# Optimization experiments

Hardware: AMD Instinct MI355X
Metric: run time of the kernel (lower is better)

## Reference

```python
import jax, jax.numpy as jnp
import numpy as np

TEMP = 0.07
DIAG_FILL = -10.0


def setup_inputs() -> dict:
    key = jax.random.key(0)
    k1, k2 = jax.random.split(key)
    N, D = 8192, 256
    feat_q = jax.random.normal(k1, (N, D), dtype=jnp.float32)
    feat_k = jax.random.normal(k2, (N, D), dtype=jnp.float32)
    return {"feat_q": feat_q, "feat_k": feat_k}


def reference(feat_q, feat_k):
    # feat_k is detached in the original module
    feat_k = jax.lax.stop_gradient(feat_k)
    N = feat_q.shape[0]

    q_norm = jnp.linalg.norm(feat_q, axis=-1, keepdims=True)  # [N,1]
    k_norm = jnp.linalg.norm(feat_k, axis=-1, keepdims=True)  # [N,1]

    # positive logits: cosine similarity of matching patches -> [N,1]
    l_pos = jnp.sum(feat_q * feat_k, axis=-1, keepdims=True) / (q_norm * k_norm)

    # negative logits: pairwise cosine similarities -> [N,N]
    l_neg = jnp.einsum('nd,md->nm', feat_q, feat_k) / (q_norm * k_norm.T)
    # mask diagonal (self pairs) with -10.0
    diag = jnp.eye(N, dtype=bool)
    l_neg = jnp.where(diag, jnp.float32(DIAG_FILL), l_neg)

    out = jnp.concatenate([l_pos, l_neg], axis=1) / TEMP  # [N, 1+N]
    # cross-entropy with target class 0, reduction='none'
    loss = jax.nn.logsumexp(out, axis=1) - out[:, 0]
    return loss
```

## Files before the change

kernel.cpp:

```cpp
#include <hip/hip_runtime.h>
#include <stdint.h>

#define N_ROWS 8192
#define DIM 256

constexpr float INV_T = 1.0f / 0.07f;
constexpr float M0    = 1.0f / 0.07f;
constexpr float LOG2E = 1.44269504088896f;
constexpr float C1    = INV_T * LOG2E;
constexpr float C0    = -M0 * LOG2E;
constexpr float KSCL  = 127.0f / 0.35f;

typedef int i32x4  __attribute__((ext_vector_type(4)));
typedef int i32x16 __attribute__((ext_vector_type(16)));

__device__ inline float fast_exp2(float x) {
    float r;
    asm("v_exp_f32 %0, %1" : "=v"(r) : "v"(x));
    return r;
}
__device__ inline int pack4(int a, int b, int c, int d) {
    return (a & 0xff) | ((b & 0xff) << 8) | ((c & 0xff) << 16) | (d << 24);
}

__global__ __launch_bounds__(256) void prep_kernel(
    const float* __restrict__ q, const float* __restrict__ k,
    int* __restrict__ qi8, int* __restrict__ ki8,
    float* __restrict__ lposT, float* __restrict__ fqs) {
    const int wid  = threadIdx.x >> 6;
    const int lane = threadIdx.x & 63;
    const int row  = blockIdx.x * 4 + wid;

    const float4 qv = *reinterpret_cast<const float4*>(q + (size_t)row * DIM + lane * 4);
    const float4 kv = *reinterpret_cast<const float4*>(k + (size_t)row * DIM + lane * 4);

    float qq = qv.x*qv.x + qv.y*qv.y + qv.z*qv.z + qv.w*qv.w;
    float kk = kv.x*kv.x + kv.y*kv.y + kv.z*kv.z + kv.w*kv.w;
    float qk = qv.x*kv.x + qv.y*kv.y + qv.z*kv.z + qv.w*kv.w;
    float qm = fmaxf(fmaxf(fabsf(qv.x), fabsf(qv.y)), fmaxf(fabsf(qv.z), fabsf(qv.w)));

    #pragma unroll
    for (int off = 32; off > 0; off >>= 1) {
        qq += __shfl_xor(qq, off, 64);
        kk += __shfl_xor(kk, off, 64);
        qk += __shfl_xor(qk, off, 64);
        qm  = fmaxf(qm, __shfl_xor(qm, off, 64));
    }
    const float iq = 1.0f / sqrtf(qq);
    const float ik = 1.0f / sqrtf(kk);

    const float ksc = ik * KSCL;
    int k0 = __float2int_rn(fminf(fmaxf(kv.x * ksc, -127.f), 127.f));
    int k1 = __float2int_rn(fminf(fmaxf(kv.y * ksc, -127.f), 127.f));
    int k2 = __float2int_rn(fminf(fmaxf(kv.z * ksc, -127.f), 127.f));
    int k3 = __float2int_rn(fminf(fmaxf(kv.w * ksc, -127.f), 127.f));
    ki8[(size_t)row * 64 + lane] = pack4(k0, k1, k2, k3);

    const float qsc = 127.0f / qm;
    int q0 = __float2int_rn(qv.x * qsc);
    int q1 = __float2int_rn(qv.y * qsc);
    int q2 = __float2int_rn(qv.z * qsc);
    int q3 = __float2int_rn(qv.w * qsc);
    qi8[(size_t)row * 64 + lane] = pack4(q0, q1, q2, q3);

    if (lane == 0) {
        lposT[row] = qk * iq * ik * INV_T;
        fqs[row] = C1 * (0.35f / (127.0f * 127.0f)) * qm * iq;
    }
}

__global__ __launch_bounds__(256, 3) void gemm_lse_kernel(
    const uint8_t* __restrict__ qi8, const uint8_t* __restrict__ ki8,
    const float* __restrict__ fqs, float* __restrict__ ps) {
    __shared__ char lds[3 * 8192];

    const int tid  = threadIdx.x;
    const int lane = tid & 63;
    const int wid  = tid >> 6;
    const int l31  = lane & 31;
    const int l5   = lane >> 5;

    const int qtile = blockIdx.x;
    const int strip = blockIdx.y;
    const int qw    = qtile * 256 + wid * 64;
    const int ks0   = strip * 512;

    auto stage = [&](int t) {
        char* dst = lds + (t % 3) * 8192;
        const int kr0 = ks0 + t * 32;
        #pragma unroll
        for (int s = 0; s < 2; ++s) {
            const int n    = wid * 2 + s;
            const int lrow = n * 8 + (lane >> 3);
            const int row  = lrow & 31;
            const int h    = lrow >> 5;
            const uint8_t* gp = ki8 + (size_t)(kr0 + row) * 256 + h * 128
                              + (((lane & 7) ^ (lrow & 7)) << 4);
            __builtin_amdgcn_global_load_lds(
                (const __attribute__((address_space(1))) void*)gp,
                (__attribute__((address_space(3))) void*)(dst + n * 1024),
                16, 0, 0);
        }
    };

    i32x4 qf[8][2];
    #pragma unroll
    for (int ks = 0; ks < 8; ++ks)
        #pragma unroll
        for (int cg = 0; cg < 2; ++cg)
            qf[ks][cg] = *reinterpret_cast<const i32x4*>(
                qi8 + (size_t)(qw + cg * 32 + l31) * 256 + ks * 32 + l5 * 16);
    const float f0 = fqs[qw + l31];
    const float f1 = fqs[qw + 32 + l31];

    stage(0);
    stage(1);

    i32x16 acc0 = {}, acc1 = {};
    float ssum0 = 0.f, ssum1 = 0.f;

    auto lda = [&](const char* src, i32x4* a) {
        #pragma unroll
        for (int ks = 0; ks < 8; ++ks) {
            const int o    = ks * 32 + l5 * 16;
            const int lrow = l31 + ((o >> 7) << 5);
            const int slot = ((o & 127) >> 4) ^ (lrow & 7);
            a[ks] = *reinterpret_cast<const i32x4*>(src + lrow * 128 + (slot << 4));
        }
    };

    auto expfrag = [&](i32x16& A, bool diag, float f, float& ss) {
        float s = 0.f;
        #pragma unroll
        for (int r = 0; r < 16; ++r) {
            float e = fast_exp2(fmaf((float)A[r], f, C0));
            if (diag && (((r & 3) + 8 * (r >> 2) + 4 * l5) == l31)) e = 0.f;
            s += e;
            A[r] = 0;
        }
        ss += s;
    };

    auto epilogue = [&](int t) {
        const int kc0 = ks0 + t * 32;
        expfrag(acc0, kc0 == qw,      f0, ssum0);
        expfrag(acc1, kc0 == qw + 32, f1, ssum1);
    };

    #pragma unroll 1
    for (int t = 0; t < 16; ++t) {
        if (t < 15) { asm volatile("s_waitcnt vmcnt(2)" ::: "memory"); }
        else        { asm volatile("s_waitcnt vmcnt(0)" ::: "memory"); }
        __builtin_amdgcn_s_barrier();
        __builtin_amdgcn_sched_barrier(0);
        if (t < 14) stage(t + 2);
        if (t > 0) epilogue(t - 1);

        const char* cur = lds + (t % 3) * 8192;
        i32x4 a[8];
        lda(cur, a);
        __builtin_amdgcn_s_setprio(1);
        #pragma unroll
        for (int ks = 0; ks < 8; ++ks) {
            acc0 = __builtin_amdgcn_mfma_i32_32x32x32_i8(a[ks], qf[ks][0], acc0, 0, 0, 0);
            acc1 = __builtin_amdgcn_mfma_i32_32x32x32_i8(a[ks], qf[ks][1], acc1, 0, 0, 0);
        }
        __builtin_amdgcn_s_setprio(0);
    }
    epilogue(15);

    ssum0 += __shfl_xor(ssum0, 32, 64);
    ssum1 += __shfl_xor(ssum1, 32, 64);
    if (lane < 32) {
        ps[(size_t)(qw + l31) * 16 + strip]      = ssum0;
        ps[(size_t)(qw + 32 + l31) * 16 + strip] = ssum1;
    }
}

__global__ __launch_bounds__(256) void finalize_kernel(
    const float* __restrict__ ps, const float* __restrict__ lposT,
    float* __restrict__ out) {
    const int row = blockIdx.x * 256 + threadIdx.x;
    float S = 0.f;
    #pragma unroll
    for (int c = 0; c < 4; ++c) {
        const float4 p = *reinterpret_cast<const float4*>(ps + (size_t)row * 16 + c * 4);
        S += p.x + p.y + p.z + p.w;
    }
    const float lp = lposT[row];
    S += __expf(lp - M0);
    out[row] = M0 + logf(S) - lp;
}

extern "C" void kernel_launch(void* const* d_in, const int* in_sizes, int n_in,
                              void* d_out, int out_size, void* d_ws, size_t ws_size,
                              hipStream_t stream) {
    const float* q = (const float*)d_in[0];
    const float* k = (const float*)d_in[1];
    float* out = (float*)d_out;

    char* ws = (char*)d_ws;
    int*   qi8 = (int*)(ws);
    int*   ki8 = (int*)(ws + (2u << 20));
    float* lpt = (float*)(ws + (4u << 20));
    float* fqs = (float*)(ws + (4u << 20) + (32u << 10));
    float* ps  = (float*)(ws + (4u << 20) + (64u << 10));

    prep_kernel<<<N_ROWS / 4, 256, 0, stream>>>(q, k, qi8, ki8, lpt, fqs);
    dim3 grid(32, 16);
    gemm_lse_kernel<<<grid, 256, 0, stream>>>((const uint8_t*)qi8, (const uint8_t*)ki8, fqs, ps);
    finalize_kernel<<<N_ROWS / 256, 256, 0, stream>>>(ps, lpt, out);
}
```

Before: 38.44 us.

## Split GEMM-LSE into single-wave blocks with private double-buffered K staging

The fused int8 GEMM plus exp-sum kernel now runs as 64-thread blocks, one wave per block, each covering 64 query rows and one key strip. Before, four waves shared a triple-buffered K tile. Each wave now loads its own K tiles into a double buffer with a new 16-slot XOR swizzle, which removes the block barrier. The exp epilogue now runs right after the MFMAs instead of being deferred one iteration. This drops barrier synchronisation and raises the number of blocks, at the cost of four times the K global-to-LDS traffic and less overlap between exp and MFMA work.

```diff
diff --git a/kernel.cpp b/kernel.cpp
--- a/kernel.cpp
+++ b/kernel.cpp
@@ -69,36 +69,29 @@
     }
 }
 
-__global__ __launch_bounds__(256, 3) void gemm_lse_kernel(
+__global__ __launch_bounds__(64) void gemm_lse_kernel(
     const uint8_t* __restrict__ qi8, const uint8_t* __restrict__ ki8,
     const float* __restrict__ fqs, float* __restrict__ ps) {
-    __shared__ char lds[3 * 8192];
-
-    const int tid  = threadIdx.x;
-    const int lane = tid & 63;
-    const int wid  = tid >> 6;
+    __shared__ char lds[2 * 8192];
+
+    const int lane = threadIdx.x;
     const int l31  = lane & 31;
     const int l5   = lane >> 5;
-
-    const int qtile = blockIdx.x;
-    const int strip = blockIdx.y;
-    const int qw    = qtile * 256 + wid * 64;
+    const int l15  = lane & 15;
+
+    const int strip = blockIdx.x;
+    const int qw    = blockIdx.y * 64;
     const int ks0   = strip * 512;
 
-    auto stage = [&](int t) {
-        char* dst = lds + (t % 3) * 8192;
+    auto stage = [&](int t, char* dst) {
         const int kr0 = ks0 + t * 32;
         #pragma unroll
-        for (int s = 0; s < 2; ++s) {
-            const int n    = wid * 2 + s;
-            const int lrow = n * 8 + (lane >> 3);
-            const int row  = lrow & 31;
-            const int h    = lrow >> 5;
-            const uint8_t* gp = ki8 + (size_t)(kr0 + row) * 256 + h * 128
-                              + (((lane & 7) ^ (lrow & 7)) << 4);
+        for (int i = 0; i < 8; ++i) {
+            const int r = i * 4 + (lane >> 4);
+            const uint8_t* gp = ki8 + (size_t)(kr0 + r) * 256 + ((l15 ^ (r & 15)) << 4);
             __builtin_amdgcn_global_load_lds(
                 (const __attribute__((address_space(1))) void*)gp,
-                (__attribute__((address_space(3))) void*)(dst + n * 1024),
+                (__attribute__((address_space(3))) void*)(dst + i * 1024),
                 16, 0, 0);
         }
     };
@@ -113,8 +106,8 @@
     const float f0 = fqs[qw + l31];
     const float f1 = fqs[qw + 32 + l31];
 
-    stage(0);
-    stage(1);
+    stage(0, lds);
+    stage(1, lds + 8192);
 
     i32x16 acc0 = {}, acc1 = {};
     float ssum0 = 0.f, ssum1 = 0.f;
@@ -122,10 +115,8 @@
     auto lda = [&](const char* src, i32x4* a) {
         #pragma unroll
         for (int ks = 0; ks < 8; ++ks) {
-            const int o    = ks * 32 + l5 * 16;
-            const int lrow = l31 + ((o >> 7) << 5);
-            const int slot = ((o & 127) >> 4) ^ (lrow & 7);
-            a[ks] = *reinterpret_cast<const i32x4*>(src + lrow * 128 + (slot << 4));
+            const int phys = (((ks << 1) | l5) ^ (l31 & 15));
+            a[ks] = *reinterpret_cast<const i32x4*>(src + l31 * 256 + (phys << 4));
         }
     };
 
@@ -141,22 +132,18 @@
         ss += s;
     };
 
-    auto epilogue = [&](int t) {
-        const int kc0 = ks0 + t * 32;
-        expfrag(acc0, kc0 == qw,      f0, ssum0);
-        expfrag(acc1, kc0 == qw + 32, f1, ssum1);
-    };
-
     #pragma unroll 1
     for (int t = 0; t < 16; ++t) {
-        if (t < 15) { asm volatile("s_waitcnt vmcnt(2)" ::: "memory"); }
-        else        { asm volatile("s_waitcnt vmcnt(0)" ::: "memory"); }
-        __builtin_amdgcn_s_barrier();
+        char* const cur = lds + (t & 1) * 8192;
+        char* const nxt = lds + ((t + 1) & 1) * 8192;
+        if (t < 15) {
+            stage(t + 1, nxt);
+            asm volatile("s_waitcnt vmcnt(8)" ::: "memory");
+        } else {
+            asm volatile("s_waitcnt vmcnt(0)" ::: "memory");
+        }
         __builtin_amdgcn_sched_barrier(0);
-        if (t < 14) stage(t + 2);
-        if (t > 0) epilogue(t - 1);
-
-        const char* cur = lds + (t % 3) * 8192;
+
         i32x4 a[8];
         lda(cur, a);
         __builtin_amdgcn_s_setprio(1);
@@ -166,8 +153,11 @@
             acc1 = __builtin_amdgcn_mfma_i32_32x32x32_i8(a[ks], qf[ks][1], acc1, 0, 0, 0);
         }
         __builtin_amdgcn_s_setprio(0);
-    }
-    epilogue(15);
+
+        const int kr0 = ks0 + t * 32;
+        expfrag(acc0, kr0 == qw,      f0, ssum0);
+        expfrag(acc1, kr0 == qw + 32, f1, ssum1);
+    }
 
     ssum0 += __shfl_xor(ssum0, 32, 64);
     ssum1 += __shfl_xor(ssum1, 32, 64);
@@ -207,7 +197,7 @@
     float* ps  = (float*)(ws + (4u << 20) + (64u << 10));
 
     prep_kernel<<<N_ROWS / 4, 256, 0, stream>>>(q, k, qi8, ki8, lpt, fqs);
-    dim3 grid(32, 16);
-    gemm_lse_kernel<<<grid, 256, 0, stream>>>((const uint8_t*)qi8, (const uint8_t*)ki8, fqs, ps);
+    dim3 grid(16, 128);
+    gemm_lse_kernel<<<grid, 64, 0, stream>>>((const uint8_t*)qi8, (const uint8_t*)ki8, fqs, ps);
     finalize_kernel<<<N_ROWS / 256, 256, 0, stream>>>(ps, lpt, out);
 }
```

New measurement: 42.28 us. +10.0%, slower.
